# Optimization experiments

Measured on AMD Instinct MI355X. Metric: run time of the kernel, lower is better.

## Reference

```python
import jax, jax.numpy as jnp
import numpy as np

N_NODES = 100000
N_EDGES = 300000
FEAT = 256
N_GRAPHS = 500
N_LAYERS = 6


def setup_inputs() -> dict:
    key = jax.random.key(0)
    ks = jax.random.split(key, 8)
    x = jax.random.normal(ks[0], (N_NODES, FEAT), dtype=jnp.float32)
    edge_index = jax.random.randint(ks[1], (2, N_EDGES), 0, N_NODES, dtype=jnp.int64)
    batch = jnp.sort(jax.random.randint(ks[2], (N_NODES,), 0, N_GRAPHS, dtype=jnp.int64))
    s = 1.0 / np.sqrt(FEAT)
    # PyG SAGEConv params: lin_l (neighbor path, with bias), lin_r (root path, no bias)
    Wl = jax.random.uniform(ks[3], (N_LAYERS, FEAT, FEAT), jnp.float32, -s, s)
    bl = jax.random.uniform(ks[4], (N_LAYERS, FEAT), jnp.float32, -s, s)
    Wr = jax.random.uniform(ks[5], (N_LAYERS, FEAT, FEAT), jnp.float32, -s, s)
    t = jnp.ones((1,), dtype=jnp.float32)  # SoftmaxAggregation learnable temperature, init 1.0
    return {"x": x, "edge_index": edge_index, "batch": batch,
            "Wl": Wl, "bl": bl, "Wr": Wr, "t": t}


def _sage_conv(x, src, dst, Wl, bl, Wr):
    # mean-aggregate source features onto destinations, then lin_l(agg) + lin_r(x)
    msg_sum = jax.ops.segment_sum(x[src], dst, num_segments=N_NODES)  # [N, F]
    deg = jax.ops.segment_sum(jnp.ones((src.shape[0],), x.dtype), dst, num_segments=N_NODES)
    mean = msg_sum / jnp.maximum(deg, 1.0)[:, None]
    return mean @ Wl.T + bl + x @ Wr.T


def _segment_softmax_aggr(x, batch, t):
    # SoftmaxAggregation: alpha = softmax(t*x over nodes per graph, per feature); out = sum(alpha*x)
    s = t * x  # [N, F]
    m = jax.ops.segment_max(s, batch, num_segments=N_GRAPHS)
    m = jnp.where(jnp.isfinite(m), m, 0.0)  # guard empty segments
    e = jnp.exp(s - m[batch])
    denom = jax.ops.segment_sum(e, batch, num_segments=N_GRAPHS)
    alpha = e / jnp.maximum(denom[batch], 1e-16)
    return jax.ops.segment_sum(alpha * x, batch, num_segments=N_GRAPHS)  # [G, F]


def reference(x, edge_index, batch, Wl, bl, Wr, t):
    src, dst = edge_index[0], edge_index[1]
    for i in range(N_LAYERS):
        x = jax.nn.relu(_sage_conv(x, src, dst, Wl[i], bl[i], Wr[i])) + x
    out = _segment_softmax_aggr(x, batch, t[0])
    return out.reshape(-1, FEAT)
```

## Files before the change

kernel.cpp:

```cpp
#include <hip/hip_runtime.h>
#include <hip/hip_bf16.h>

#define N_NODES  100000
#define N_EDGES  300000
#define FEAT     256
#define N_GRAPHS 500
#define N_LAYERS 6
#define SCAN_B   1024

typedef __attribute__((ext_vector_type(8))) short v8s;
typedef __attribute__((ext_vector_type(4))) float v4f;

__device__ __forceinline__ unsigned short f2bf(float f) {
    unsigned u = __float_as_uint(f);
    unsigned r = u + 0x7fffu + ((u >> 16) & 1u);
    return (unsigned short)(r >> 16);
}
__device__ __forceinline__ float bf2f(unsigned short b) {
    return __uint_as_float(((unsigned)b) << 16);
}

__device__ __forceinline__ void gload16(const ushort* g, ushort* l) {
    __builtin_amdgcn_global_load_lds((const __attribute__((address_space(1))) void*)g,
                                     (__attribute__((address_space(3))) void*)l,
                                     16, 0, 0);
}

__global__ __launch_bounds__(256) void init_kernel(const float* __restrict__ x,
                                                   ushort* __restrict__ xb) {
    int i = blockIdx.x * 256 + threadIdx.x;
    if ((size_t)i * 4 >= (size_t)N_NODES * FEAT) return;
    float4 v = ((const float4*)x)[i];
    ((ushort4*)xb)[i] = make_ushort4(f2bf(v.x), f2bf(v.y), f2bf(v.z), f2bf(v.w));
}

__global__ __launch_bounds__(256) void wconv_kernel(const float* __restrict__ Wl,
                                                    const float* __restrict__ Wr,
                                                    ushort* __restrict__ wlb,
                                                    ushort* __restrict__ wrb) {
    int i = blockIdx.x * 256 + threadIdx.x;
    if ((size_t)i * 4 >= (size_t)N_LAYERS * FEAT * FEAT) return;
    float4 a = ((const float4*)Wl)[i];
    float4 b = ((const float4*)Wr)[i];
    ((ushort4*)wlb)[i] = make_ushort4(f2bf(a.x), f2bf(a.y), f2bf(a.z), f2bf(a.w));
    ((ushort4*)wrb)[i] = make_ushort4(f2bf(b.x), f2bf(b.y), f2bf(b.z), f2bf(b.w));
}


__global__ __launch_bounds__(256) void hist_kernel(const int* __restrict__ dst,
                                                   unsigned* __restrict__ degu) {
    int e = blockIdx.x * 256 + threadIdx.x;
    if (e < N_EDGES) atomicAdd(&degu[dst[e]], 1u);
}

__global__ __launch_bounds__(SCAN_B) void scan_blocks(const unsigned* __restrict__ degu,
                                                      unsigned* __restrict__ excl,
                                                      unsigned* __restrict__ bsum) {
    __shared__ unsigned tmp[SCAN_B];
    int i = blockIdx.x * SCAN_B + threadIdx.x;
    unsigned v = (i < N_NODES) ? degu[i] : 0u;
    tmp[threadIdx.x] = v;
    __syncthreads();
    for (int off = 1; off < SCAN_B; off <<= 1) {
        unsigned add = (threadIdx.x >= off) ? tmp[threadIdx.x - off] : 0u;
        __syncthreads();
        tmp[threadIdx.x] += add;
        __syncthreads();
    }
    if (i < N_NODES) excl[i] = tmp[threadIdx.x] - v;
    if (threadIdx.x == SCAN_B - 1) bsum[blockIdx.x] = tmp[SCAN_B - 1];
}

__global__ void scan_tops(unsigned* __restrict__ bsum, int nb) {
    unsigned run = 0;
    for (int b = 0; b < nb; ++b) { unsigned t = bsum[b]; bsum[b] = run; run += t; }
}

__global__ __launch_bounds__(256) void finalize_rowptr(const unsigned* __restrict__ excl,
                                                       const unsigned* __restrict__ bsum,
                                                       unsigned* __restrict__ rowptr,
                                                       unsigned* __restrict__ cursor) {
    int i = blockIdx.x * 256 + threadIdx.x;
    if (i < N_NODES) {
        unsigned v = excl[i] + bsum[i / SCAN_B];
        rowptr[i] = v;
        cursor[i] = v;
    }
    if (i == N_NODES) rowptr[N_NODES] = N_EDGES;
}

__global__ __launch_bounds__(256) void scatter_kernel(const int* __restrict__ ei,
                                                      unsigned* __restrict__ cursor,
                                                      unsigned* __restrict__ col) {
    int e = blockIdx.x * 256 + threadIdx.x;
    if (e >= N_EDGES) return;
    int d = ei[N_EDGES + e];
    unsigned p = atomicAdd(&cursor[d], 1u);
    col[p] = (unsigned)ei[e];
}

__global__ __launch_bounds__(256) void bounds_kernel(const int* __restrict__ batch,
                                                     unsigned* __restrict__ gs,
                                                     unsigned* __restrict__ ge) {
    int i = blockIdx.x * 256 + threadIdx.x;
    if (i >= N_NODES) return;
    int g = batch[i];
    int gp = (i == 0) ? -1 : batch[i - 1];
    if (g != gp) gs[g] = (unsigned)i;
    int gn = (i == N_NODES - 1) ? -1 : batch[i + 1];
    if (g != gn) ge[g] = (unsigned)(i + 1);
}

#define CPAD  264

__global__ __launch_bounds__(512, 4) void gemm_kernel(
        const unsigned* __restrict__ rowptr,
        const unsigned* __restrict__ col,
        const ushort* __restrict__ xb,
        const ushort* __restrict__ B0,
        const ushort* __restrict__ B1,
        const float*  __restrict__ bias,
        ushort* __restrict__ xbn) {
    __shared__ ushort lds[36864];
    ushort* Ms  = lds;
    ushort* Bs0 = lds + 16384;
    ushort* Bs1 = lds + 24576;
    ushort* Xs0 = lds + 32768;
    ushort* Xs1 = lds + 34816;
    ushort* Cs  = lds;

    const int tid  = threadIdx.x;
    const int lane = tid & 63;
    const int wid  = tid >> 6;
    const int row0 = blockIdx.x * 64;

    const int pB0  = tid >> 3;
    const int w0B0 = ((tid & 7) ^ (pB0 & 7)) << 4;
    const int rB0  = 2 * pB0 + (w0B0 >> 6);
    const int cbB0 = w0B0 & 63;
    const int c1   = tid + 512;
    const int pB1  = c1 >> 3;
    const int w0B1 = ((c1 & 7) ^ (pB1 & 7)) << 4;
    const int rB1  = 2 * pB1 + (w0B1 >> 6);
    const int cbB1 = w0B1 & 63;
    const int pX   = tid >> 3;
    const int w0X  = ((tid & 7) ^ (pX & 7)) << 4;
    int rX = row0 + 2 * pX + (w0X >> 6);
    rX = rX < N_NODES ? rX : N_NODES - 1;
    const int cbX  = w0X & 63;

    #define STAGE_B(bufPtr, kt) do {                                              \
        const ushort* Bsrc = ((kt) < 8) ? B0 : B1;                                \
        const int kb = ((kt) & 7) * 32;                                           \
        gload16(Bsrc + (size_t)rB0 * FEAT + kb + (cbB0 >> 1), (bufPtr) + tid * 8);\
        gload16(Bsrc + (size_t)rB1 * FEAT + kb + (cbB1 >> 1), (bufPtr) + (size_t)c1 * 8); \
    } while (0)

    #define STAGE_X(bufPtr, kt) do {                                              \
        if (tid < 256) {                                                          \
            const int kb = ((kt) & 7) * 32;                                       \
            gload16(xb + (size_t)rX * FEAT + kb + (cbX >> 1), (bufPtr) + tid * 8);\
        }                                                                          \
    } while (0)

    STAGE_B(Bs0, 0);

    {
        const int h   = lane >> 5;
        const int l32 = lane & 31;
        #pragma unroll 1
        for (int p = 0; p < 4; ++p) {
            const int nl = wid * 8 + p * 2 + h;
            const int node = row0 + nl;
            unsigned s = 0, e = 0;
            if (node < N_NODES) { s = rowptr[node]; e = rowptr[node + 1]; }
            float a0=0.f,a1=0.f,a2=0.f,a3=0.f,a4=0.f,a5=0.f,a6=0.f,a7=0.f;
            #pragma unroll 1
            for (unsigned base = s; base < e; base += 32) {
                unsigned idx = base + (unsigned)l32;
                int cv = (idx < e) ? (int)col[idx] : 0;
                int n = (int)(e - base); n = n > 32 ? 32 : n;
                #pragma unroll 1
                for (int j = 0; j < n; ++j) {
                    unsigned src = (unsigned)__shfl(cv, (h << 5) + j);
                    v8s v = *(const v8s*)(xb + (size_t)src * FEAT + l32 * 8);
                    a0 += bf2f((ushort)v[0]); a1 += bf2f((ushort)v[1]);
                    a2 += bf2f((ushort)v[2]); a3 += bf2f((ushort)v[3]);
                    a4 += bf2f((ushort)v[4]); a5 += bf2f((ushort)v[5]);
                    a6 += bf2f((ushort)v[6]); a7 += bf2f((ushort)v[7]);
                }
            }
            float r = 1.0f / fmaxf((float)(e - s), 1.0f);
            v8s o;
            o[0]=(short)f2bf(a0*r); o[1]=(short)f2bf(a1*r);
            o[2]=(short)f2bf(a2*r); o[3]=(short)f2bf(a3*r);
            o[4]=(short)f2bf(a4*r); o[5]=(short)f2bf(a5*r);
            o[6]=(short)f2bf(a6*r); o[7]=(short)f2bf(a7*r);
            *(v8s*)((char*)Ms + nl * 512 + ((l32 * 16) ^ ((nl & 7) << 4))) = o;
        }
    }
    __syncthreads();

    v4f acc[4][2] = {};
    const int fr  = lane & 15;
    const int cbk = (lane >> 4) << 4;

    #define FRAG(basePtr, row) \
        (*(const v8s*)((const char*)(basePtr) + (((row) >> 1) * 128 + \
            ((((row) & 1) << 6) + cbk) ^ ((((row) >> 1) & 7) << 4))))

    #define AFRAG_M(kt, row) \
        (*(const v8s*)((const char*)Ms + (row) * 512 + \
            ((((kt) << 6) + cbk) ^ (((row) & 7) << 4))))

    #define PHASE(kt, APART) do {                                                 \
        v8s a[4], b[2];                                                           \
        _Pragma("unroll")                                                         \
        for (int i = 0; i < 4; ++i) a[i] = APART;                                 \
        {                                                                          \
            const ushort* bp = ((kt) & 1) ? Bs1 : Bs0;                            \
            _Pragma("unroll")                                                     \
            for (int j = 0; j < 2; ++j) b[j] = FRAG(bp, wid * 32 + j * 16 + fr);  \
        }                                                                          \
        _Pragma("unroll")                                                         \
        for (int i = 0; i < 4; ++i)                                               \
            _Pragma("unroll")                                                     \
            for (int j = 0; j < 2; ++j)                                           \
                acc[i][j] = __builtin_amdgcn_mfma_f32_16x16x32_bf16(a[i], b[j], acc[i][j], 0, 0, 0); \
    } while (0)

    #pragma unroll
    for (int kt = 0; kt < 8; ++kt) {
        STAGE_B((kt & 1) ? Bs0 : Bs1, kt + 1);
        if (kt == 7) STAGE_X(Xs0, 8);
        PHASE(kt, AFRAG_M(kt, i * 16 + fr));
        __syncthreads();
    }
    #pragma unroll
    for (int kt = 8; kt < 16; ++kt) {
        if (kt < 15) {
            STAGE_B((kt & 1) ? Bs0 : Bs1, kt + 1);
            STAGE_X((kt & 1) ? Xs0 : Xs1, kt + 1);
        }
        const ushort* xp = (kt & 1) ? Xs1 : Xs0;
        PHASE(kt, FRAG(xp, i * 16 + fr));
        __syncthreads();
    }
    #undef PHASE
    #undef AFRAG_M

    {
        const int orow = (lane >> 4) * 4;
        const int ocol = lane & 15;
        #pragma unroll
        for (int j = 0; j < 2; ++j) {
            int colg = wid * 32 + j * 16 + ocol;
            float bv = bias[colg];
            #pragma unroll
            for (int i = 0; i < 4; ++i) {
                int rl = i * 16 + orow;
                #pragma unroll
                for (int r = 0; r < 4; ++r)
                    Cs[(rl + r) * CPAD + colg] = f2bf(fmaxf(acc[i][j][r] + bv, 0.0f));
            }
        }
    }
    __builtin_amdgcn_s_barrier();
    {
        int rl  = tid >> 3;
        int row = row0 + rl;
        #pragma unroll
        for (int it = 0; it < 4; ++it) {
            int c0 = (tid & 7) * 8 + it * 64;
            v8s y = *(const v8s*)(Cs + rl * CPAD + c0);
            if (row < N_NODES) {
                v8s xv = *(const v8s*)(xb + (size_t)row * FEAT + c0);
                v8s o;
                #pragma unroll
                for (int k = 0; k < 8; ++k)
                    o[k] = (short)f2bf(bf2f((ushort)y[k]) + bf2f((ushort)xv[k]));
                *(v8s*)(xbn + (size_t)row * FEAT + c0) = o;
            }
        }
    }
    #undef STAGE_B
    #undef STAGE_X
    #undef FRAG
}

__global__ __launch_bounds__(512) void smax_kernel(const ushort* __restrict__ xb,
                                                   const unsigned* __restrict__ gs,
                                                   const unsigned* __restrict__ ge,
                                                   const float* __restrict__ t,
                                                   float* __restrict__ out) {
    __shared__ float sm[16 * 256];
    __shared__ float sd[16 * 256];
    __shared__ float sa[16 * 256];
    const int g   = blockIdx.x;
    const unsigned s = gs[g], e = ge[g];
    const float tv2 = t[0] * 1.44269504f;
    const int tid = threadIdx.x;
    const int c   = tid >> 5;
    const int f8  = (tid & 31) * 8;

    float m[8], den[8], acc[8];
    #pragma unroll
    for (int k = 0; k < 8; ++k) { m[k] = -INFINITY; den[k] = 0.f; acc[k] = 0.f; }

    if (s < e) {
        for (unsigned n = s + c; n < e; n += 16) {
            v8s v = *(const v8s*)(xb + (size_t)n * FEAT + f8);
            #pragma unroll
            for (int k = 0; k < 8; ++k) {
                float xv = bf2f((ushort)v[k]);
                float s2 = xv * tv2;
                float mn = fmaxf(m[k], s2);
                float sc = exp2f(m[k] - mn);
                float w  = exp2f(s2 - mn);
                den[k] = den[k] * sc + w;
                acc[k] = acc[k] * sc + w * xv;
                m[k] = mn;
            }
        }
    }
    #pragma unroll
    for (int k = 0; k < 8; ++k) {
        sm[c * 256 + f8 + k] = m[k];
        sd[c * 256 + f8 + k] = den[k];
        sa[c * 256 + f8 + k] = acc[k];
    }
    __syncthreads();
    if (tid < 256) {
        if (s < e) {
            const int f = tid;
            float M = -INFINITY;
            #pragma unroll
            for (int cc = 0; cc < 16; ++cc) M = fmaxf(M, sm[cc * 256 + f]);
            float D = 0.f, A = 0.f;
            #pragma unroll
            for (int cc = 0; cc < 16; ++cc) {
                float w = exp2f(sm[cc * 256 + f] - M);
                D += sd[cc * 256 + f] * w;
                A += sa[cc * 256 + f] * w;
            }
            out[(size_t)g * FEAT + tid] = A / fmaxf(D, 1e-16f);
        } else {
            out[(size_t)g * FEAT + tid] = 0.f;
        }
    }
}

extern "C" void kernel_launch(void* const* d_in, const int* in_sizes, int n_in,
                              void* d_out, int out_size, void* d_ws, size_t ws_size,
                              hipStream_t stream) {
    const float* x     = (const float*)d_in[0];
    const int*   ei    = (const int*)d_in[1];
    const int*   batch = (const int*)d_in[2];
    const float* Wl    = (const float*)d_in[3];
    const float* bl    = (const float*)d_in[4];
    const float* Wr    = (const float*)d_in[5];
    const float* t     = (const float*)d_in[6];
    float* out = (float*)d_out;

    const size_t NF2 = (size_t)N_NODES * FEAT * 2;
    const size_t WSZ = (size_t)N_LAYERS * FEAT * FEAT * 2;

    char* ws = (char*)d_ws;
    size_t off = 0;
    ushort* xb0   = (ushort*)(ws + off); off += NF2;
    ushort* xb1   = (ushort*)(ws + off); off += NF2;
    ushort* wlb   = (ushort*)(ws + off); off += WSZ;
    ushort* wrb   = (ushort*)(ws + off); off += WSZ;
    unsigned* degu   = (unsigned*)(ws + off); off += (size_t)N_NODES * 4;
    unsigned* excl   = (unsigned*)(ws + off); off += (size_t)N_NODES * 4;
    unsigned* bsum   = (unsigned*)(ws + off); off += 128 * 4;
    unsigned* rowptr = (unsigned*)(ws + off); off += (size_t)(N_NODES + 1) * 4;
    unsigned* cursor = (unsigned*)(ws + off); off += (size_t)N_NODES * 4;
    unsigned* col    = (unsigned*)(ws + off); off += (size_t)N_EDGES * 4;
    unsigned* gs     = (unsigned*)(ws + off); off += (size_t)N_GRAPHS * 4;
    unsigned* ge     = (unsigned*)(ws + off); off += (size_t)N_GRAPHS * 4;

    hipMemsetAsync(degu, 0, (size_t)N_NODES * 4, stream);
    hipMemsetAsync(gs, 0xFF, (size_t)N_GRAPHS * 4, stream);
    hipMemsetAsync(ge, 0, (size_t)N_GRAPHS * 4, stream);

    init_kernel<<<(N_NODES * FEAT / 4 + 255) / 256, 256, 0, stream>>>(x, xb0);
    wconv_kernel<<<(N_LAYERS * FEAT * FEAT / 4 + 255) / 256, 256, 0, stream>>>(Wl, Wr, wlb, wrb);

    const int NB_SCAN = (N_NODES + SCAN_B - 1) / SCAN_B;
    hist_kernel<<<(N_EDGES + 255) / 256, 256, 0, stream>>>(ei + N_EDGES, degu);
    scan_blocks<<<NB_SCAN, SCAN_B, 0, stream>>>(degu, excl, bsum);
    scan_tops<<<1, 1, 0, stream>>>(bsum, NB_SCAN);
    finalize_rowptr<<<(N_NODES + 256) / 256, 256, 0, stream>>>(excl, bsum, rowptr, cursor);
    scatter_kernel<<<(N_EDGES + 255) / 256, 256, 0, stream>>>(ei, cursor, col);

    bounds_kernel<<<(N_NODES + 255) / 256, 256, 0, stream>>>(batch, gs, ge);

    ushort* cur = xb0;
    ushort* nxt = xb1;
    for (int l = 0; l < N_LAYERS; ++l) {
        gemm_kernel<<<dim3((N_NODES + 63) / 64), 512, 0, stream>>>(
            rowptr, col, cur,
            wlb + (size_t)l * FEAT * FEAT, wrb + (size_t)l * FEAT * FEAT,
            bl + (size_t)l * FEAT, nxt);
        ushort* tmp = cur; cur = nxt; nxt = tmp;
    }

    smax_kernel<<<N_GRAPHS, 512, 0, stream>>>(cur, gs, ge, t, out);
}
```

Before: 605.5 us.

## Batch neighbor gathers four at a time and restructure GEMM K-loop barriers

The mean-aggregation gather now handles four neighbors per iteration. It issues four independent row loads and masks out-of-range lanes with 0/1 multipliers instead of loading one row at a time, and the per-node loop is unrolled by 2. The goal is more outstanding memory requests to hide gather latency. The two GEMM K-loops are merged into one loop. It places an explicit vmcnt wait plus barrier at the top of each step rather than a __syncthreads at the end, and raises wave priority around the MFMA block. A barrier is added before the epilogue writes to shared memory. The cost is extra registers and some redundant loads for the masked tail lanes.

Result: faster. 548.4 us (-9.4%).

```diff
diff --git a/kernel.cpp b/kernel.cpp
--- a/kernel.cpp
+++ b/kernel.cpp
@@ -168,7 +168,7 @@
     {
         const int h   = lane >> 5;
         const int l32 = lane & 31;
-        #pragma unroll 1
+        #pragma unroll 2
         for (int p = 0; p < 4; ++p) {
             const int nl = wid * 8 + p * 2 + h;
             const int node = row0 + nl;
@@ -181,13 +181,31 @@
                 int cv = (idx < e) ? (int)col[idx] : 0;
                 int n = (int)(e - base); n = n > 32 ? 32 : n;
                 #pragma unroll 1
-                for (int j = 0; j < n; ++j) {
-                    unsigned src = (unsigned)__shfl(cv, (h << 5) + j);
-                    v8s v = *(const v8s*)(xb + (size_t)src * FEAT + l32 * 8);
-                    a0 += bf2f((ushort)v[0]); a1 += bf2f((ushort)v[1]);
-                    a2 += bf2f((ushort)v[2]); a3 += bf2f((ushort)v[3]);
-                    a4 += bf2f((ushort)v[4]); a5 += bf2f((ushort)v[5]);
-                    a6 += bf2f((ushort)v[6]); a7 += bf2f((ushort)v[7]);
+                for (int j = 0; j < n; j += 4) {
+                    int nj = n - 1;
+                    int l0 = (h << 5) + j;
+                    int l1 = (h << 5) + (j + 1 < n ? j + 1 : nj);
+                    int l2 = (h << 5) + (j + 2 < n ? j + 2 : nj);
+                    int l3 = (h << 5) + (j + 3 < n ? j + 3 : nj);
+                    float m1 = (j + 1 < n) ? 1.f : 0.f;
+                    float m2 = (j + 2 < n) ? 1.f : 0.f;
+                    float m3 = (j + 3 < n) ? 1.f : 0.f;
+                    unsigned s0 = (unsigned)__shfl(cv, l0);
+                    unsigned s1 = (unsigned)__shfl(cv, l1);
+                    unsigned s2 = (unsigned)__shfl(cv, l2);
+                    unsigned s3 = (unsigned)__shfl(cv, l3);
+                    v8s v0 = *(const v8s*)(xb + (size_t)s0 * FEAT + l32 * 8);
+                    v8s v1 = *(const v8s*)(xb + (size_t)s1 * FEAT + l32 * 8);
+                    v8s v2 = *(const v8s*)(xb + (size_t)s2 * FEAT + l32 * 8);
+                    v8s v3 = *(const v8s*)(xb + (size_t)s3 * FEAT + l32 * 8);
+                    a0 += bf2f((ushort)v0[0]) + m1*bf2f((ushort)v1[0]) + m2*bf2f((ushort)v2[0]) + m3*bf2f((ushort)v3[0]);
+                    a1 += bf2f((ushort)v0[1]) + m1*bf2f((ushort)v1[1]) + m2*bf2f((ushort)v2[1]) + m3*bf2f((ushort)v3[1]);
+                    a2 += bf2f((ushort)v0[2]) + m1*bf2f((ushort)v1[2]) + m2*bf2f((ushort)v2[2]) + m3*bf2f((ushort)v3[2]);
+                    a3 += bf2f((ushort)v0[3]) + m1*bf2f((ushort)v1[3]) + m2*bf2f((ushort)v2[3]) + m3*bf2f((ushort)v3[3]);
+                    a4 += bf2f((ushort)v0[4]) + m1*bf2f((ushort)v1[4]) + m2*bf2f((ushort)v2[4]) + m3*bf2f((ushort)v3[4]);
+                    a5 += bf2f((ushort)v0[5]) + m1*bf2f((ushort)v1[5]) + m2*bf2f((ushort)v2[5]) + m3*bf2f((ushort)v3[5]);
+                    a6 += bf2f((ushort)v0[6]) + m1*bf2f((ushort)v1[6]) + m2*bf2f((ushort)v2[6]) + m3*bf2f((ushort)v3[6]);
+                    a7 += bf2f((ushort)v0[7]) + m1*bf2f((ushort)v1[7]) + m2*bf2f((ushort)v2[7]) + m3*bf2f((ushort)v3[7]);
                 }
             }
             float r = 1.0f / fmaxf((float)(e - s), 1.0f);
@@ -213,42 +231,42 @@
         (*(const v8s*)((const char*)Ms + (row) * 512 + \
             ((((kt) << 6) + cbk) ^ (((row) & 7) << 4))))
 
-    #define PHASE(kt, APART) do {                                                 \
-        v8s a[4], b[2];                                                           \
-        _Pragma("unroll")                                                         \
-        for (int i = 0; i < 4; ++i) a[i] = APART;                                 \
-        {                                                                          \
-            const ushort* bp = ((kt) & 1) ? Bs1 : Bs0;                            \
-            _Pragma("unroll")                                                     \
-            for (int j = 0; j < 2; ++j) b[j] = FRAG(bp, wid * 32 + j * 16 + fr);  \
-        }                                                                          \
-        _Pragma("unroll")                                                         \
-        for (int i = 0; i < 4; ++i)                                               \
-            _Pragma("unroll")                                                     \
-            for (int j = 0; j < 2; ++j)                                           \
-                acc[i][j] = __builtin_amdgcn_mfma_f32_16x16x32_bf16(a[i], b[j], acc[i][j], 0, 0, 0); \
-    } while (0)
-
     #pragma unroll
-    for (int kt = 0; kt < 8; ++kt) {
-        STAGE_B((kt & 1) ? Bs0 : Bs1, kt + 1);
-        if (kt == 7) STAGE_X(Xs0, 8);
-        PHASE(kt, AFRAG_M(kt, i * 16 + fr));
-        __syncthreads();
-    }
-    #pragma unroll
-    for (int kt = 8; kt < 16; ++kt) {
+    for (int kt = 0; kt < 16; ++kt) {
+        if (kt > 0) {
+            asm volatile("s_waitcnt vmcnt(0)" ::: "memory");
+            __builtin_amdgcn_s_barrier();
+        }
         if (kt < 15) {
             STAGE_B((kt & 1) ? Bs0 : Bs1, kt + 1);
-            STAGE_X((kt & 1) ? Xs0 : Xs1, kt + 1);
-        }
-        const ushort* xp = (kt & 1) ? Xs1 : Xs0;
-        PHASE(kt, FRAG(xp, i * 16 + fr));
-        __syncthreads();
-    }
-    #undef PHASE
+            if (kt == 7) STAGE_X(Xs0, 8);
+            if (kt >= 8) STAGE_X((kt & 1) ? Xs0 : Xs1, kt + 1);
+        }
+        v8s a[4], b[2];
+        if (kt < 8) {
+            #pragma unroll
+            for (int i = 0; i < 4; ++i) a[i] = AFRAG_M(kt, i * 16 + fr);
+        } else {
+            const ushort* xp = (kt & 1) ? Xs1 : Xs0;
+            #pragma unroll
+            for (int i = 0; i < 4; ++i) a[i] = FRAG(xp, i * 16 + fr);
+        }
+        {
+            const ushort* bp = (kt & 1) ? Bs1 : Bs0;
+            #pragma unroll
+            for (int j = 0; j < 2; ++j) b[j] = FRAG(bp, wid * 32 + j * 16 + fr);
+        }
+        __builtin_amdgcn_s_setprio(1);
+        #pragma unroll
+        for (int i = 0; i < 4; ++i)
+            #pragma unroll
+            for (int j = 0; j < 2; ++j)
+                acc[i][j] = __builtin_amdgcn_mfma_f32_16x16x32_bf16(a[i], b[j], acc[i][j], 0, 0, 0);
+        __builtin_amdgcn_s_setprio(0);
+    }
     #undef AFRAG_M
 
+    __builtin_amdgcn_s_barrier();
     {
         const int orow = (lane >> 4) * 4;
         const int ocol = lane & 15;
@@ -265,7 +283,7 @@
             }
         }
     }
-    __builtin_amdgcn_s_barrier();
+    __syncthreads();
     {
         int rl  = tid >> 3;
         int row = row0 + rl;
```
